# Performance work log

Hardware: AMD Instinct MI355X
Metric: run time of the kernel (lower is better)

Reference implementation:

```python
import jax, jax.numpy as jnp
import numpy as np

DIM = 1024
HEADS = 16
DIM_HEAD = 64
B, N = 2, 2048
EPS_NORM = 1e-12  # F.normalize clamp


def setup_inputs() -> dict:
    key = jax.random.key(0)
    k1, k2, k3 = jax.random.split(key, 3)
    x = jax.random.normal(k1, (B, N, DIM), dtype=jnp.float32)
    gamma = jnp.ones((DIM,), dtype=jnp.float32)
    w_qkv = jax.random.normal(k2, (DIM, 3 * HEADS * DIM_HEAD), dtype=jnp.float32) * (DIM ** -0.5)
    w_out = jax.random.normal(k3, (HEADS * DIM_HEAD, DIM), dtype=jnp.float32) * (DIM ** -0.5)
    return {"x": x, "gamma": gamma, "w_qkv": w_qkv, "w_out": w_out}


def reference(x, gamma, w_qkv, w_out):
    b, n, dim = x.shape
    h, dh = HEADS, DIM_HEAD
    # RMSNorm: F.normalize(x, dim=-1) * sqrt(dim) * gamma
    norm = jnp.maximum(jnp.linalg.norm(x, axis=-1, keepdims=True), EPS_NORM)
    normed = x / norm * (dim ** 0.5) * gamma
    # qkv projection (no bias)
    qkv = normed @ w_qkv  # [b, n, 3*h*dh]
    qkv = qkv.reshape(b, n, 3, h, dh)
    q = qkv[:, :, 0].transpose(0, 2, 1, 3)  # [b, h, n, dh]
    k = qkv[:, :, 1].transpose(0, 2, 1, 3)
    v = qkv[:, :, 2].transpose(0, 2, 1, 3)
    q = q * (dh ** -0.5)
    # attention scores
    sim = jnp.einsum('bhid,bhjd->bhij', q, k)
    mask_value = -jnp.finfo(sim.dtype).max
    # causal mask: triu with offset j - i + 1 (here i == j == n -> offset 1)
    causal_mask = jnp.triu(jnp.ones((n, n), dtype=bool), 1)
    sim = jnp.where(causal_mask, mask_value, sim)
    attn = jax.nn.softmax(sim, axis=-1)
    out = jnp.einsum('bhij,bhjd->bhid', attn, v)
    out = out.transpose(0, 2, 1, 3).reshape(b, n, h * dh)
    return out @ w_out
```

## Files before the change

### kernel.cpp

```cpp
#include <hip/hip_runtime.h>
#include <hip/hip_bf16.h>

typedef unsigned short u16;
using bf16x8 = __attribute__((ext_vector_type(8))) short;
using f32x4  = __attribute__((ext_vector_type(4))) float;
using f32x16 = __attribute__((ext_vector_type(16))) float;
using u32x4  = __attribute__((ext_vector_type(4))) unsigned int;

constexpr int B_ = 2, N_ = 2048, DIM_ = 1024, H_ = 16, DH_ = 64;
constexpr int M_ = B_ * N_;
constexpr int NCQ = 3 * H_ * DH_;

__device__ inline u16 f2bf(float f) {
  union { float f; unsigned u; } v{f};
  unsigned r = v.u + 0x7FFF + ((v.u >> 16) & 1);
  return (u16)(r >> 16);
}

__device__ __forceinline__ void st_pair(u16* p0, u16* p1, float a, float b) {
  unsigned w;
  asm("v_cvt_pk_bf16_f32 %0, %1, %2" : "=v"(w) : "v"(a), "v"(b));
  *p0 = (u16)w;
  *p1 = (u16)(w >> 16);
}

__device__ __forceinline__ void gload16(const u16* g, u16* l) {
  __builtin_amdgcn_global_load_lds(
      (const __attribute__((address_space(1))) unsigned int*)g,
      (__attribute__((address_space(3))) unsigned int*)l, 16, 0, 0);
}

__global__ void __launch_bounds__(256) rmsnorm_kernel(const float* __restrict__ x,
                                                      const float* __restrict__ gamma,
                                                      u16* __restrict__ out) {
  int row = blockIdx.x;
  int t = threadIdx.x;
  const float4 v = reinterpret_cast<const float4*>(x + (size_t)row * DIM_)[t];
  float ss = v.x * v.x + v.y * v.y + v.z * v.z + v.w * v.w;
#pragma unroll
  for (int o = 32; o; o >>= 1) ss += __shfl_down(ss, o, 64);
  __shared__ float partial[4];
  int wid = t >> 6, lane = t & 63;
  if (lane == 0) partial[wid] = ss;
  __syncthreads();
  float tot = partial[0] + partial[1] + partial[2] + partial[3];
  float norm = fmaxf(sqrtf(tot), 1e-12f);
  float scale = 32.0f / norm;
  const float4 g = reinterpret_cast<const float4*>(gamma)[t];
  ushort4 o4;
  o4.x = f2bf(v.x * scale * g.x);
  o4.y = f2bf(v.y * scale * g.y);
  o4.z = f2bf(v.z * scale * g.z);
  o4.w = f2bf(v.w * scale * g.w);
  reinterpret_cast<ushort4*>(out + (size_t)row * DIM_)[t] = o4;
}

__global__ void __launch_bounds__(256) transpose_w_kernel(const float* __restrict__ W,
                                                          u16* __restrict__ WT,
                                                          int K, int Nc) {
  __shared__ float tile[32][33];
  int bc = blockIdx.x * 32;
  int bk = blockIdx.y * 32;
  int tx = threadIdx.x & 31, ty = threadIdx.x >> 5;
#pragma unroll
  for (int r = ty; r < 32; r += 8)
    tile[r][tx] = W[(size_t)(bk + r) * Nc + bc + tx];
  __syncthreads();
#pragma unroll
  for (int r = ty; r < 32; r += 8)
    WT[(size_t)(bc + r) * K + bk + tx] = f2bf(tile[tx][r]);
}

template <int MODE>
__global__ void __launch_bounds__(256) gemm2_kernel(const u16* __restrict__ A,
                                                    const u16* __restrict__ BT,
                                                    void* __restrict__ Cv,
                                                    u16* __restrict__ q_s,
                                                    u16* __restrict__ k_s,
                                                    u16* __restrict__ vt,
                                                    int M, int Nc, int K) {
  __shared__ alignas(16) u16 smem[16384];
  int tid = threadIdx.x;
  int lane = tid & 63, wid = tid >> 6;
  int lr = lane & 15, g = lane >> 4;
  int am0 = (wid >> 1) * 64;
  int bn0 = (wid & 1) * 64;
  int rbase_a = blockIdx.y * 128;
  int rbase_b = blockIdx.x * 128;

  int lineo = tid >> 3;
  int p = tid & 7;
  f32x4 acc[4][4] = {};

#define GSTAGE(base_, src_, rb_, k0_) do {                                           \
    _Pragma("unroll")                                                                \
    for (int c = 0; c < 2; c++) {                                                    \
      int line = c * 32 + lineo;                                                     \
      int sp = p ^ (line & 7);                                                       \
      int row = 2 * line + (sp >> 2);                                                \
      int j = sp & 3;                                                                \
      gload16(src_ + (size_t)(rb_ + row) * K + (k0_) + j * 8,                        \
              (base_) + c * 2048 + wid * 512);                                       \
    }                                                                                \
  } while (0)

#define STAGE(ib_, k0_) do {                                                         \
    GSTAGE(smem + (ib_) * 4096, A, rbase_a, k0_);                                    \
    GSTAGE(smem + 8192 + (ib_) * 4096, BT, rbase_b, k0_);                            \
  } while (0)

  int steps = K >> 5;
  STAGE(0, 0);
  for (int t = 0; t < steps; ++t) {
    int ibuf = t & 1;
    if (t + 1 < steps) {
      STAGE(ibuf ^ 1, (t + 1) * 32);
      asm volatile("s_waitcnt vmcnt(4)" ::: "memory");
    } else {
      asm volatile("s_waitcnt vmcnt(0)" ::: "memory");
    }
    __builtin_amdgcn_s_barrier();
    __builtin_amdgcn_sched_barrier(0);

    const char* ab = (const char*)(smem + ibuf * 4096);
    const char* bb = (const char*)(smem + 8192 + ibuf * 4096);
    bf16x8 a[4], b[4];
#pragma unroll
    for (int mi = 0; mi < 4; mi++) {
      int row = am0 + mi * 16 + lr;
      int byte = (row >> 1) * 128 + ((((row & 1) << 2) + g) ^ ((row >> 1) & 7)) * 16;
      a[mi] = *reinterpret_cast<const bf16x8*>(ab + byte);
    }
#pragma unroll
    for (int ni = 0; ni < 4; ni++) {
      int row = bn0 + ni * 16 + lr;
      int byte = (row >> 1) * 128 + ((((row & 1) << 2) + g) ^ ((row >> 1) & 7)) * 16;
      b[ni] = *reinterpret_cast<const bf16x8*>(bb + byte);
    }
#pragma unroll
    for (int mi = 0; mi < 4; mi++)
#pragma unroll
      for (int ni = 0; ni < 4; ni++)
        acc[mi][ni] = __builtin_amdgcn_mfma_f32_16x16x32_bf16(a[mi], b[ni], acc[mi][ni], 0, 0, 0);

    __builtin_amdgcn_sched_barrier(0);
    __builtin_amdgcn_s_barrier();
  }

  int orow = g * 4;
  if (MODE == 1) {
#pragma unroll
    for (int mi = 0; mi < 4; mi++)
#pragma unroll
      for (int ni = 0; ni < 4; ni++)
#pragma unroll
        for (int r = 0; r < 4; r++) {
          int row = rbase_a + am0 + 16 * mi + orow + r;
          int col = rbase_b + bn0 + 16 * ni + lr;
          ((float*)Cv)[(size_t)row * Nc + col] = acc[mi][ni][r];
        }
  } else {
    int colbase = rbase_b + bn0;
    int region = colbase >> 10;
    int head = (colbase >> 6) & 15;
    const float QS = 0.125f * 1.4426950408889634f;
    if (region < 2) {
#pragma unroll
      for (int mi = 0; mi < 4; mi++)
#pragma unroll
        for (int ni = 0; ni < 4; ni++)
#pragma unroll
          for (int r = 0; r < 4; r += 2) {
            int row = rbase_a + am0 + 16 * mi + orow + r;
            int n = row & 2047, bb_ = row >> 11;
            float v0 = acc[mi][ni][r], v1 = acc[mi][ni][r + 1];
            size_t d0 = ((size_t)(bb_ * 16 + head) * 2048 + n) * 64 + 16 * ni + lr;
            if (region == 0)
              st_pair(q_s + d0, q_s + d0 + 64, v0 * QS, v1 * QS);
            else
              st_pair(k_s + d0, k_s + d0 + 64, v0, v1);
          }
    } else {
      u16* tlds = smem + wid * 4096;
      int n_base = (rbase_a + am0) & 2047;
      int bq = (rbase_a + am0) >> 11;
#pragma unroll
      for (int mi = 0; mi < 4; mi++)
#pragma unroll
        for (int ni = 0; ni < 4; ni++) {
          int n_loc = mi * 16 + orow;
          int dh_loc = ni * 16 + lr;
          unsigned w0, w1;
          asm("v_cvt_pk_bf16_f32 %0, %1, %2"
              : "=v"(w0) : "v"(acc[mi][ni][0]), "v"(acc[mi][ni][1]));
          asm("v_cvt_pk_bf16_f32 %0, %1, %2"
              : "=v"(w1) : "v"(acc[mi][ni][2]), "v"(acc[mi][ni][3]));
          int byte = dh_loc * 128 + ((n_loc * 2) ^ ((dh_loc & 7) << 4));
          uint2 val; val.x = w0; val.y = w1;
          *reinterpret_cast<uint2*>((char*)tlds + byte) = val;
        }
#pragma unroll
      for (int it = 0; it < 8; it++) {
        int dh_loc = it * 8 + (lane >> 3);
        int n8 = (lane & 7) * 8;
        int byte = dh_loc * 128 + ((n8 * 2) ^ ((dh_loc & 7) << 4));
        bf16x8 v = *reinterpret_cast<const bf16x8*>((const char*)tlds + byte);
        size_t dst = ((size_t)(bq * 16 + head) * 64 + dh_loc) * 2048 + n_base + n8;
        *reinterpret_cast<bf16x8*>(vt + dst) = v;
      }
    }
  }
#undef STAGE
#undef GSTAGE
}

__global__ void __launch_bounds__(256) attn9_kernel(const u16* __restrict__ q_s,
                                                    const u16* __restrict__ k_s,
                                                    const u16* __restrict__ vt,
                                                    u16* __restrict__ ao) {
  __shared__ alignas(16) u16 smem[16384];
  u16* kb0 = smem;
  u16* vb0 = smem + 8192;
  int tid = threadIdx.x;
  int lane = tid & 63, wid = tid >> 6;
  int q31 = lane & 31, hi = lane >> 5;
  int strip = wid >> 1, myhalf = wid & 1;
  int blk = blockIdx.x;
  int bh = blk & 31;
  int s = blk >> 5;
  int u = s & 7, gq = s >> 3;
  int j = (gq == 0) ? (31 - u) : (gq == 1) ? (16 + u) : (gq == 2) ? (15 - u) : u;
  int b = bh >> 4, h = bh & 15;
  const u16* qp = q_s + (size_t)bh * N_ * DH_;
  const u16* kp = k_s + (size_t)bh * N_ * DH_;
  const u16* vp = vt + (size_t)bh * DH_ * N_;
  int q0w = j * 64 + strip * 32;
  int qi = q0w + q31;
  int steps = j + 1;

  bf16x8 qf[4];
#pragma unroll
  for (int c = 0; c < 4; c++)
    qf[c] = *reinterpret_cast<const bf16x8*>(qp + (size_t)(q0w + q31) * 64 + c * 16 + hi * 8);

  f32x16 o0 = {}, o1 = {};
  float lsum = 0.f;

  int srow = lane >> 3;
  int scol = (lane & 7) ^ srow;
  int c0 = wid * 2, c1 = c0 + 1;

#define STAGE(ibuf_, kv0_) do {                                                              \
    gload16(kp + (size_t)((kv0_) + c0 * 8 + srow) * 64 + scol * 8,                           \
            kb0 + (ibuf_) * 4096 + c0 * 512);                                                \
    gload16(kp + (size_t)((kv0_) + c1 * 8 + srow) * 64 + scol * 8,                           \
            kb0 + (ibuf_) * 4096 + c1 * 512);                                                \
    gload16(vp + (size_t)(c0 * 8 + srow) * N_ + (kv0_) + scol * 8,                           \
            vb0 + (ibuf_) * 4096 + c0 * 512);                                                \
    gload16(vp + (size_t)(c1 * 8 + srow) * N_ + (kv0_) + scol * 8,                           \
            vb0 + (ibuf_) * 4096 + c1 * 512);                                                \
  } while (0)

  STAGE(0, 0);

  for (int t = 0; t < steps; ++t) {
    int ibuf = t & 1;
    if (t + 1 < steps) {
      STAGE(ibuf ^ 1, (t + 1) * 64);
      asm volatile("s_waitcnt vmcnt(4)" ::: "memory");
    } else {
      asm volatile("s_waitcnt vmcnt(0)" ::: "memory");
    }
    __builtin_amdgcn_s_barrier();
    __builtin_amdgcn_sched_barrier(0);

    const u16* kb = kb0 + ibuf * 4096;
    const u16* vb = vb0 + ibuf * 4096;
    int kv = t * 64 + myhalf * 32;
    if (kv <= q0w + 31) {
      f32x16 st = {};
      int krow = myhalf * 32 + q31;
      int ksw = (krow & 7) << 4;
      __builtin_amdgcn_s_setprio(1);
#pragma unroll
      for (int c = 0; c < 4; c++) {
        bf16x8 kf = *reinterpret_cast<const bf16x8*>(
            (const char*)kb + krow * 128 + (((c * 2 + hi) * 16) ^ ksw));
        st = __builtin_amdgcn_mfma_f32_32x32x16_bf16(kf, qf[c], st, 0, 0, 0);
      }
      __builtin_amdgcn_s_setprio(0);
      float p[16];
      bool diag = (kv + 31 > q0w);
      if (diag) {
#pragma unroll
        for (int r = 0; r < 16; r++) {
          int key = kv + (r & 3) + 8 * (r >> 2) + 4 * hi;
          float e = __builtin_amdgcn_exp2f(st[r]);
          p[r] = (key > qi) ? 0.f : e;
        }
      } else {
#pragma unroll
        for (int r = 0; r < 16; r++) p[r] = __builtin_amdgcn_exp2f(st[r]);
      }
#pragma unroll
      for (int r = 0; r < 16; r++) lsum += p[r];
      unsigned cw0[4], cw1[4];
#pragma unroll
      for (int jq2 = 0; jq2 < 4; jq2++) {
        asm("v_cvt_pk_bf16_f32 %0, %1, %2" : "=v"(cw0[jq2]) : "v"(p[4 * jq2]), "v"(p[4 * jq2 + 1]));
        asm("v_cvt_pk_bf16_f32 %0, %1, %2" : "=v"(cw1[jq2]) : "v"(p[4 * jq2 + 2]), "v"(p[4 * jq2 + 3]));
      }
#pragma unroll
      for (int kc = 0; kc < 2; kc++) {
        unsigned c0a = cw0[2 * kc], c0b = cw0[2 * kc + 1];
        unsigned c1a = cw1[2 * kc], c1b = cw1[2 * kc + 1];
        unsigned sel0 = hi ? c0a : c0b;
        unsigned sel1 = hi ? c1a : c1b;
        unsigned r0 = (unsigned)__shfl_xor((int)sel0, 32, 64);
        unsigned r1 = (unsigned)__shfl_xor((int)sel1, 32, 64);
        u32x4 w;
        w[0] = hi ? r0 : c0a;
        w[1] = hi ? r1 : c1a;
        w[2] = hi ? c0b : r0;
        w[3] = hi ? c1b : r1;
        bf16x8 pa = __builtin_bit_cast(bf16x8, w);
        int slot = (myhalf * 4 + kc * 2 + hi) * 16;
        int vsw = (q31 & 7) << 4;
        bf16x8 vf0 = *reinterpret_cast<const bf16x8*>(
            (const char*)vb + q31 * 128 + (slot ^ vsw));
        bf16x8 vf1 = *reinterpret_cast<const bf16x8*>(
            (const char*)vb + (32 + q31) * 128 + (slot ^ vsw));
        __builtin_amdgcn_s_setprio(1);
        o0 = __builtin_amdgcn_mfma_f32_32x32x16_bf16(pa, vf0, o0, 0, 0, 0);
        o1 = __builtin_amdgcn_mfma_f32_32x32x16_bf16(pa, vf1, o1, 0, 0, 0);
        __builtin_amdgcn_s_setprio(0);
      }
    }
    __builtin_amdgcn_sched_barrier(0);
    __builtin_amdgcn_s_barrier();
  }

  __syncthreads();
  float lc = lsum + __shfl_xor(lsum, 32, 64);
  float* cb = (float*)smem;
  int pr = wid >> 1;
  if (myhalf) {
#pragma unroll
    for (int r = 0; r < 16; r++) {
      cb[pr * 2048 + r * 64 + lane] = o0[r];
      cb[pr * 2048 + (16 + r) * 64 + lane] = o1[r];
    }
    cb[4096 + pr * 64 + lane] = lc;
  }
  __syncthreads();
  if (!myhalf) {
#pragma unroll
    for (int r = 0; r < 16; r++) {
      o0[r] += cb[pr * 2048 + r * 64 + lane];
      o1[r] += cb[pr * 2048 + (16 + r) * 64 + lane];
    }
    float ltot = fmaxf(lc + cb[4096 + pr * 64 + lane], 1e-30f);
    float linv = 1.0f / ltot;
#pragma unroll
    for (int r = 0; r < 16; r += 2) {
      int qrow0 = (r & 3) + 8 * (r >> 2) + 4 * hi;
      float li0 = __shfl(linv, qrow0, 64);
      float li1 = __shfl(linv, qrow0 + 1, 64);
      size_t base0 = (size_t)(b * N_ + q0w + qrow0) * 1024 + h * 64;
      st_pair(ao + base0 + q31, ao + base0 + 1024 + q31, o0[r] * li0, o0[r + 1] * li1);
      st_pair(ao + base0 + 32 + q31, ao + base0 + 1024 + 32 + q31, o1[r] * li0, o1[r + 1] * li1);
    }
  }
#undef STAGE
}

extern "C" void kernel_launch(void* const* d_in, const int* in_sizes, int n_in,
                              void* d_out, int out_size, void* d_ws, size_t ws_size,
                              hipStream_t stream) {
  const float* x = (const float*)d_in[0];
  const float* gamma = (const float*)d_in[1];
  const float* w_qkv = (const float*)d_in[2];
  const float* w_out = (const float*)d_in[3];
  float* out = (float*)d_out;

  char* p = (char*)d_ws;
  u16* normed = (u16*)p; p += (size_t)M_ * DIM_ * 2;
  u16* wt_qkv = (u16*)p; p += (size_t)NCQ * DIM_ * 2;
  u16* wt_out = (u16*)p; p += (size_t)DIM_ * DIM_ * 2;
  u16* k_s = (u16*)p;    p += (size_t)M_ * DIM_ * 2;
  u16* vt = (u16*)p;     p += (size_t)M_ * DIM_ * 2;
  u16* q_s = (u16*)p;    p += (size_t)M_ * DIM_ * 2;
  u16* ao = (u16*)p;     p += (size_t)M_ * DIM_ * 2;

  hipLaunchKernelGGL(rmsnorm_kernel, dim3(M_), dim3(256), 0, stream, x, gamma, normed);
  hipLaunchKernelGGL(transpose_w_kernel, dim3(NCQ / 32, DIM_ / 32), dim3(256), 0, stream,
                     w_qkv, wt_qkv, DIM_, NCQ);
  hipLaunchKernelGGL(transpose_w_kernel, dim3(DIM_ / 32, DIM_ / 32), dim3(256), 0, stream,
                     w_out, wt_out, DIM_, DIM_);
  hipLaunchKernelGGL(gemm2_kernel<2>, dim3(NCQ / 128, M_ / 128), dim3(256), 0, stream,
                     normed, wt_qkv, nullptr, q_s, k_s, vt, M_, NCQ, DIM_);
  hipLaunchKernelGGL(attn9_kernel, dim3(B_ * H_ * (N_ / 64)), dim3(256), 0, stream,
                     q_s, k_s, vt, ao);
  hipLaunchKernelGGL(gemm2_kernel<1>, dim3(DIM_ / 128, M_ / 128), dim3(256), 0, stream,
                     ao, wt_out, (void*)out, nullptr, nullptr, nullptr, M_, DIM_, DIM_);
}
```

Before: 102.9 us.

## Merge prep kernels into one launch and remap GEMM workgroups for XCD locality

Folds the RMSNorm kernel and both weight-transpose kernels into a single prep kernel that branches on block index, which removes two kernel launches and the gaps between them. Both GEMM launches move to a 1D grid whose block index is permuted so that consecutive tiles land on the same XCD (index mod 8), aiming for better L2 reuse of A/B tiles. The remap hardcodes 32 row tiles (M=4096/128), so it depends on the fixed problem shape.

```diff
diff --git a/kernel.cpp b/kernel.cpp
--- a/kernel.cpp
+++ b/kernel.cpp
@@ -30,45 +30,58 @@
       (__attribute__((address_space(3))) unsigned int*)l, 16, 0, 0);
 }
 
-__global__ void __launch_bounds__(256) rmsnorm_kernel(const float* __restrict__ x,
-                                                      const float* __restrict__ gamma,
-                                                      u16* __restrict__ out) {
-  int row = blockIdx.x;
+__global__ void __launch_bounds__(256) prep_kernel(const float* __restrict__ x,
+                                                   const float* __restrict__ gamma,
+                                                   const float* __restrict__ wq,
+                                                   const float* __restrict__ wo,
+                                                   u16* __restrict__ normed,
+                                                   u16* __restrict__ wtq,
+                                                   u16* __restrict__ wto) {
+  __shared__ float tile[32][33];
+  int blk = blockIdx.x;
   int t = threadIdx.x;
-  const float4 v = reinterpret_cast<const float4*>(x + (size_t)row * DIM_)[t];
-  float ss = v.x * v.x + v.y * v.y + v.z * v.z + v.w * v.w;
-#pragma unroll
-  for (int o = 32; o; o >>= 1) ss += __shfl_down(ss, o, 64);
-  __shared__ float partial[4];
-  int wid = t >> 6, lane = t & 63;
-  if (lane == 0) partial[wid] = ss;
-  __syncthreads();
-  float tot = partial[0] + partial[1] + partial[2] + partial[3];
-  float norm = fmaxf(sqrtf(tot), 1e-12f);
-  float scale = 32.0f / norm;
-  const float4 g = reinterpret_cast<const float4*>(gamma)[t];
-  ushort4 o4;
-  o4.x = f2bf(v.x * scale * g.x);
-  o4.y = f2bf(v.y * scale * g.y);
-  o4.z = f2bf(v.z * scale * g.z);
-  o4.w = f2bf(v.w * scale * g.w);
-  reinterpret_cast<ushort4*>(out + (size_t)row * DIM_)[t] = o4;
-}
-
-__global__ void __launch_bounds__(256) transpose_w_kernel(const float* __restrict__ W,
-                                                          u16* __restrict__ WT,
-                                                          int K, int Nc) {
-  __shared__ float tile[32][33];
-  int bc = blockIdx.x * 32;
-  int bk = blockIdx.y * 32;
-  int tx = threadIdx.x & 31, ty = threadIdx.x >> 5;
-#pragma unroll
-  for (int r = ty; r < 32; r += 8)
-    tile[r][tx] = W[(size_t)(bk + r) * Nc + bc + tx];
-  __syncthreads();
-#pragma unroll
-  for (int r = ty; r < 32; r += 8)
-    WT[(size_t)(bc + r) * K + bk + tx] = f2bf(tile[tx][r]);
+  if (blk < M_) {
+    const float4 v = reinterpret_cast<const float4*>(x + (size_t)blk * DIM_)[t];
+    float ss = v.x * v.x + v.y * v.y + v.z * v.z + v.w * v.w;
+#pragma unroll
+    for (int o = 32; o; o >>= 1) ss += __shfl_down(ss, o, 64);
+    int wid = t >> 6, lane = t & 63;
+    if (lane == 0) tile[0][wid] = ss;
+    __syncthreads();
+    float tot = tile[0][0] + tile[0][1] + tile[0][2] + tile[0][3];
+    float norm = fmaxf(sqrtf(tot), 1e-12f);
+    float scale = 32.0f / norm;
+    const float4 g = reinterpret_cast<const float4*>(gamma)[t];
+    ushort4 o4;
+    o4.x = f2bf(v.x * scale * g.x);
+    o4.y = f2bf(v.y * scale * g.y);
+    o4.z = f2bf(v.z * scale * g.z);
+    o4.w = f2bf(v.w * scale * g.w);
+    reinterpret_cast<ushort4*>(normed + (size_t)blk * DIM_)[t] = o4;
+  } else {
+    const float* W;
+    u16* WT;
+    int Nc, bc, bk;
+    if (blk < M_ + 3072) {
+      int idx = blk - M_;
+      W = wq; WT = wtq; Nc = NCQ;
+      bc = (idx % 96) * 32;
+      bk = (idx / 96) * 32;
+    } else {
+      int idx = blk - (M_ + 3072);
+      W = wo; WT = wto; Nc = DIM_;
+      bc = (idx & 31) * 32;
+      bk = (idx >> 5) * 32;
+    }
+    int tx = t & 31, ty = t >> 5;
+#pragma unroll
+    for (int r = ty; r < 32; r += 8)
+      tile[r][tx] = W[(size_t)(bk + r) * Nc + bc + tx];
+    __syncthreads();
+#pragma unroll
+    for (int r = ty; r < 32; r += 8)
+      WT[(size_t)(bc + r) * DIM_ + bk + tx] = f2bf(tile[tx][r]);
+  }
 }
 
 template <int MODE>
@@ -85,8 +98,12 @@
   int lr = lane & 15, g = lane >> 4;
   int am0 = (wid >> 1) * 64;
   int bn0 = (wid & 1) * 64;
-  int rbase_a = blockIdx.y * 128;
-  int rbase_b = blockIdx.x * 128;
+  int nwg = gridDim.x;
+  int lwg = (blockIdx.x & 7) * (nwg >> 3) + (blockIdx.x >> 3);
+  int by = lwg & 31;
+  int bx = lwg >> 5;
+  int rbase_a = by * 128;
+  int rbase_b = bx * 128;
 
   int lineo = tid >> 3;
   int p = tid & 7;
@@ -392,15 +409,12 @@
   u16* q_s = (u16*)p;    p += (size_t)M_ * DIM_ * 2;
   u16* ao = (u16*)p;     p += (size_t)M_ * DIM_ * 2;
 
-  hipLaunchKernelGGL(rmsnorm_kernel, dim3(M_), dim3(256), 0, stream, x, gamma, normed);
-  hipLaunchKernelGGL(transpose_w_kernel, dim3(NCQ / 32, DIM_ / 32), dim3(256), 0, stream,
-                     w_qkv, wt_qkv, DIM_, NCQ);
-  hipLaunchKernelGGL(transpose_w_kernel, dim3(DIM_ / 32, DIM_ / 32), dim3(256), 0, stream,
-                     w_out, wt_out, DIM_, DIM_);
-  hipLaunchKernelGGL(gemm2_kernel<2>, dim3(NCQ / 128, M_ / 128), dim3(256), 0, stream,
+  hipLaunchKernelGGL(prep_kernel, dim3(M_ + 3072 + 1024), dim3(256), 0, stream,
+                     x, gamma, w_qkv, w_out, normed, wt_qkv, wt_out);
+  hipLaunchKernelGGL(gemm2_kernel<2>, dim3((NCQ / 128) * (M_ / 128)), dim3(256), 0, stream,
                      normed, wt_qkv, nullptr, q_s, k_s, vt, M_, NCQ, DIM_);
   hipLaunchKernelGGL(attn9_kernel, dim3(B_ * H_ * (N_ / 64)), dim3(256), 0, stream,
                      q_s, k_s, vt, ao);
-  hipLaunchKernelGGL(gemm2_kernel<1>, dim3(DIM_ / 128, M_ / 128), dim3(256), 0, stream,
+  hipLaunchKernelGGL(gemm2_kernel<1>, dim3((DIM_ / 128) * (M_ / 128)), dim3(256), 0, stream,
                      ao, wt_out, (void*)out, nullptr, nullptr, nullptr, M_, DIM_, DIM_);
 }
```

Measured after the change: 100.2 us, median of 3. -2.6%, faster.
